# Optimization experiments

Measured on AMD Instinct MI355X. Metric: run time of the kernel, lower is better.

Reference implementation:

```python
import jax, jax.numpy as jnp
import numpy as np

B, D_IN = 32, 1024
A, N_PER = 4, 2048
N = A * N_PER
OUT_DIM = 11
THRESHOLD = 0.05
SELF_MASK, CROSS_MASK = 0.8, 0.1


def setup_inputs() -> dict:
    key = jax.random.key(0)
    ks = jax.random.split(key, 8)
    return {
        "x": jax.random.normal(ks[0], (B, D_IN), dtype=jnp.float32),
        "Z0": jax.random.normal(ks[1], (B, A, N_PER), dtype=jnp.float32),
        "receptors_w": jax.random.normal(ks[2], (N, D_IN), dtype=jnp.float32) * 0.02,
        "receptors_b": jax.random.normal(ks[3], (N,), dtype=jnp.float32) * 0.02,
        "synapses_w": jax.random.normal(ks[4], (N, N), dtype=jnp.float32) * 0.02,
        "synapses_b": jax.random.normal(ks[5], (N,), dtype=jnp.float32) * 0.02,
        "output_lobe_w": jax.random.normal(ks[6], (OUT_DIM, N), dtype=jnp.float32) * 0.02,
        "output_lobe_b": jax.random.normal(ks[7], (OUT_DIM,), dtype=jnp.float32) * 0.02,
        "area_idx": jnp.arange(N, dtype=jnp.int64).reshape(A, N_PER),
    }


def reference(x, Z0, receptors_w, receptors_b, synapses_w, synapses_b,
              output_lobe_w, output_lobe_b, area_idx):
    # area_idx: [A, n] partition of neurons into areas; perm: [N]
    perm = area_idx.reshape(-1)
    b = x.shape[0]

    # stimulus[i] = F.linear(x, receptors_w[idx_i], receptors_b[idx_i]),
    # computed for all areas at once then reshaped to per-area blocks.
    stim_flat = x @ receptors_w.T + receptors_b          # [B, N]
    stim = stim_flat[:, perm].reshape(b, A, N_PER)        # [B, A, n]

    # threshold gate per source area: |Z|.mean() > threshold (predicated)
    gate = (jnp.mean(jnp.abs(Z0), axis=(0, 2)) > THRESHOLD).astype(Z0.dtype)  # [A]

    # per-(out,in)-block synapse weights with clamped mask scale
    Wp = synapses_w[perm][:, perm].reshape(A, N_PER, A, N_PER)  # [A,n,A,n]
    scale = jnp.where(jnp.eye(A, dtype=bool), SELF_MASK, CROSS_MASK)  # [A,A]
    Weff = Wp * scale[:, None, :, None]

    # Z_next[out] = sum_in gate[in] * (Z[in] @ Weff[out,:,in,:].T) + gate[out]*bias[out]
    Zg = Z0 * gate[None, :, None]                         # [B, A, n]
    Znext = jnp.einsum('onam,bam->bon', Weff, Zg)         # [B, A, n]
    bias_blocks = synapses_b[perm].reshape(A, N_PER)      # diagonal-block bias
    Znext = Znext + gate[:, None] * bias_blocks           # fires with in==out gate

    Znew = jnp.tanh(Znext + stim)                         # [B, A, n]

    # scatter per-area state back into flat neuron order
    Z_flat = jnp.zeros((b, N), dtype=Znew.dtype).at[:, perm].set(Znew.reshape(b, N))

    raw = Z_flat @ output_lobe_w.T + output_lobe_b        # [B, 11]
    logits = raw[:, :10]
    out_gate = jax.nn.sigmoid(raw[:, 10])
    return logits, out_gate
```

## Files before the change

kernel.cpp:

```cpp
#include <hip/hip_runtime.h>
#include <math.h>

#define BATCH 32
#define DIN   1024
#define NAREA 4
#define NPER  2048
#define NTOT  8192
#define KC    256
#define RPB   16
#define SYN_CHUNKS 32
#define ALL_CHUNKS 36

typedef __attribute__((address_space(1))) const unsigned int gu32_t;
typedef __attribute__((address_space(3))) unsigned int su32_t;

__device__ __forceinline__ void load_lds16(const float* g, float* l) {
  __builtin_amdgcn_global_load_lds((gu32_t*)g, (su32_t*)l, 16, 0, 0);
}

__global__ void k_gate(const float* __restrict__ Z0, float* __restrict__ gsum) {
  const int a = blockIdx.x >> 3;
  const int slice = blockIdx.x & 7;
  const int tid = threadIdx.x;
  float s = 0.f;
#pragma unroll
  for (int it = 0; it < 8; ++it) {
    const int idx = it * 256 + tid;
    const int b = slice * 4 + (idx >> 9);
    const int n4 = idx & 511;
    const float4 z = *(const float4*)(Z0 + (size_t)b * NTOT + a * NPER + n4 * 4);
    s += fabsf(z.x) + fabsf(z.y) + fabsf(z.z) + fabsf(z.w);
  }
#pragma unroll
  for (int off = 32; off > 0; off >>= 1) s += __shfl_down(s, off);
  __shared__ float wsum[4];
  if ((tid & 63) == 0) wsum[tid >> 6] = s;
  __syncthreads();
  if (tid == 0) atomicAdd(&gsum[a], wsum[0] + wsum[1] + wsum[2] + wsum[3]);
}

__launch_bounds__(256, 2)
__global__ void k_main(const float* __restrict__ x,  const float* __restrict__ Z0,
                       const float* __restrict__ Rw, const float* __restrict__ rbias,
                       const float* __restrict__ Sw, const float* __restrict__ sbias,
                       const float* __restrict__ gsum, float* __restrict__ Zn) {
  __shared__ __align__(16) float zs[2][BATCH][KC];
  const int tid = threadIdx.x;
  const int w = tid >> 6, lane = tid & 63;
  const int r0 = blockIdx.x * RPB;
  const int o = r0 / NPER;
  const int rw0 = r0 + w * 4;

  float gate[NAREA], coeff[NAREA];
#pragma unroll
  for (int a = 0; a < NAREA; ++a) {
    gate[a] = (gsum[a] * (1.f / (BATCH * NPER)) > 0.05f) ? 1.f : 0.f;
    coeff[a] = gate[a] * ((a == o) ? 0.8f : 0.1f);
  }

  float acc[4][BATCH];
#pragma unroll
  for (int i = 0; i < 4; ++i)
#pragma unroll
    for (int b = 0; b < BATCH; ++b) acc[i][b] = 0.f;

  auto stage = [&](int kc, int buf) {
    const float* X; int stride, k0;
    if (kc < SYN_CHUNKS) { X = Z0; stride = NTOT; k0 = kc * KC; }
    else                 { X = x;  stride = DIN;  k0 = (kc - SYN_CHUNKS) * KC; }
#pragma unroll
    for (int i = 0; i < 8; ++i) {
      const int b = w * 8 + i;
      load_lds16(X + (size_t)b * stride + k0 + lane * 4, &zs[buf][b][0]);
    }
  };

  stage(0, 0);
  for (int kc = 0; kc < ALL_CHUNKS; ++kc) {
    const int buf = kc & 1;
    __syncthreads();
    if (kc + 1 < ALL_CHUNKS) stage(kc + 1, buf ^ 1);

    const float* Wm; int strideW, k0; float s;
    if (kc < SYN_CHUNKS) { Wm = Sw; strideW = NTOT; k0 = kc * KC; s = coeff[kc >> 3]; }
    else                 { Wm = Rw; strideW = DIN;  k0 = (kc - SYN_CHUNKS) * KC; s = 1.f; }

    float4 wv[4];
#pragma unroll
    for (int i = 0; i < 4; ++i)
      wv[i] = *(const float4*)(Wm + (size_t)(rw0 + i) * strideW + k0 + lane * 4);
#pragma unroll
    for (int i = 0; i < 4; ++i) { wv[i].x *= s; wv[i].y *= s; wv[i].z *= s; wv[i].w *= s; }

#pragma unroll
    for (int b = 0; b < BATCH; ++b) {
      const float4 z = *(const float4*)&zs[buf][b][lane * 4];
#pragma unroll
      for (int i = 0; i < 4; ++i) {
        acc[i][b] = fmaf(wv[i].x, z.x, acc[i][b]);
        acc[i][b] = fmaf(wv[i].y, z.y, acc[i][b]);
        acc[i][b] = fmaf(wv[i].z, z.z, acc[i][b]);
        acc[i][b] = fmaf(wv[i].w, z.w, acc[i][b]);
      }
    }
  }

  float (*L)[64] = reinterpret_cast<float (*)[64]>(&zs[0][0][0]);
  const float gate_o = gate[o];
#pragma unroll
  for (int h = 0; h < 2; ++h) {
    __syncthreads();
#pragma unroll
    for (int i = 0; i < 4; ++i)
#pragma unroll
      for (int bb = 0; bb < 16; ++bb)
        L[(w * 4 + i) * 16 + bb][lane] = acc[i][h * 16 + bb];
    __syncthreads();
#pragma unroll
    for (int step = 0; step < 6; ++step) {
      const int off = 32 >> step;
      for (int idx = tid; idx < (off << 8); idx += 256) {
        const int out = idx >> (5 - step);
        const int l = idx & (off - 1);
        L[out][l] += L[out][l + off];
      }
      __syncthreads();
    }
    const int r = r0 + (tid >> 4);
    const int b = h * 16 + (tid & 15);
    const float v = L[tid][0] + rbias[r] + gate_o * sbias[r];
    Zn[(size_t)r * BATCH + b] = tanhf(v);
  }
}

__global__ void k_proj(const float* __restrict__ Zn, const float* __restrict__ olw,
                       float* __restrict__ raw) {
  const int j = blockIdx.x >> 4;
  const int rs = blockIdx.x & 15;
  const int tid = threadIdx.x;
  const int b = tid & 31, stripe = tid >> 5;
  const int rbase = rs * 512 + stripe * 64;
  float a = 0.f;
#pragma unroll
  for (int rr = 0; rr < 64; ++rr) {
    const int r = rbase + rr;
    a = fmaf(olw[j * NTOT + r], Zn[(size_t)r * BATCH + b], a);
  }
  __shared__ float red[8][33];
  red[stripe][b] = a;
  __syncthreads();
  if (stripe == 0) {
    float v = 0.f;
#pragma unroll
    for (int s2 = 0; s2 < 8; ++s2) v += red[s2][b];
    atomicAdd(&raw[j * BATCH + b], v);
  }
}

__global__ void k_fin(const float* __restrict__ raw, const float* __restrict__ olb,
                      float* __restrict__ out) {
  const int t = threadIdx.x;
  if (t < 352) {
    const int j = t >> 5, b = t & 31;
    const float v = raw[j * BATCH + b] + olb[j];
    if (j < 10) out[b * 10 + j] = v;
    else        out[320 + b] = 1.f / (1.f + expf(-v));
  }
}

extern "C" void kernel_launch(void* const* d_in, const int* in_sizes, int n_in,
                              void* d_out, int out_size, void* d_ws, size_t ws_size,
                              hipStream_t stream) {
  const float* x    = (const float*)d_in[0];
  const float* Z0   = (const float*)d_in[1];
  const float* Rw   = (const float*)d_in[2];
  const float* rb_  = (const float*)d_in[3];
  const float* Sw   = (const float*)d_in[4];
  const float* sb_  = (const float*)d_in[5];
  const float* olw  = (const float*)d_in[6];
  const float* olb  = (const float*)d_in[7];

  float* ws   = (float*)d_ws;
  float* gsum = ws;
  float* raw  = ws + 8;
  float* Zn   = ws + 512;

  hipMemsetAsync(d_ws, 0, 512 * sizeof(float), stream);
  k_gate<<<32, 256, 0, stream>>>(Z0, gsum);
  k_main<<<NTOT / RPB, 256, 0, stream>>>(x, Z0, Rw, rb_, Sw, sb_, gsum, Zn);
  k_proj<<<11 * 16, 256, 0, stream>>>(Zn, olw, raw);
  k_fin<<<1, 384, 0, stream>>>(raw, olb, (float*)d_out);
}
```

Measured before the change: 430.6 us.

## Use bf16 MFMA for the fused synapse and receptor GEMM with pre-gated bf16 activations

Adds a prep kernel that applies the per-area gate to Z0, concatenates it with x, and converts the result to a bf16 activation matrix. The main kernel now runs 16x16x32 bf16 MFMAs on a 512-thread block, with each wave taking interleaved K chunks. Weights are scaled and converted to bf16 in registers, and the per-wave partial sums are reduced through LDS. This replaces the FP32 FMA loop and its LDS staging with matrix-core work, at the cost of bf16 precision and an extra kernel launch.

```diff
diff --git a/kernel.cpp b/kernel.cpp
--- a/kernel.cpp
+++ b/kernel.cpp
@@ -3,19 +3,18 @@
 
 #define BATCH 32
 #define DIN   1024
-#define NAREA 4
 #define NPER  2048
 #define NTOT  8192
-#define KC    256
-#define RPB   16
-#define SYN_CHUNKS 32
-#define ALL_CHUNKS 36
+#define KTOT  9216
+#define NCHUNK 288
 
-typedef __attribute__((address_space(1))) const unsigned int gu32_t;
-typedef __attribute__((address_space(3))) unsigned int su32_t;
+typedef __attribute__((ext_vector_type(8))) short short8;
+typedef __attribute__((ext_vector_type(4))) float f32x4;
 
-__device__ __forceinline__ void load_lds16(const float* g, float* l) {
-  __builtin_amdgcn_global_load_lds((gu32_t*)g, (su32_t*)l, 16, 0, 0);
+__device__ __forceinline__ unsigned short f2bf(float f) {
+  unsigned u = __float_as_uint(f);
+  u += 0x7FFF + ((u >> 16) & 1);
+  return (unsigned short)(u >> 16);
 }
 
 __global__ void k_gate(const float* __restrict__ Z0, float* __restrict__ gsum) {
@@ -39,98 +38,93 @@
   if (tid == 0) atomicAdd(&gsum[a], wsum[0] + wsum[1] + wsum[2] + wsum[3]);
 }
 
-__launch_bounds__(256, 2)
-__global__ void k_main(const float* __restrict__ x,  const float* __restrict__ Z0,
-                       const float* __restrict__ Rw, const float* __restrict__ rbias,
+__global__ void k_prep(const float* __restrict__ Z0, const float* __restrict__ x,
+                       const float* __restrict__ gsum, unsigned short* __restrict__ zg) {
+  const int idx = blockIdx.x * 256 + threadIdx.x;
+  const int b = idx / (KTOT / 4);
+  const int k = (idx % (KTOT / 4)) * 4;
+  float4 v; float g;
+  if (k < NTOT) {
+    v = *(const float4*)(Z0 + (size_t)b * NTOT + k);
+    g = (gsum[k >> 11] * (1.f / (BATCH * NPER)) > 0.05f) ? 1.f : 0.f;
+  } else {
+    v = *(const float4*)(x + (size_t)b * DIN + (k - NTOT));
+    g = 1.f;
+  }
+  ushort4 o;
+  o.x = f2bf(v.x * g); o.y = f2bf(v.y * g);
+  o.z = f2bf(v.z * g); o.w = f2bf(v.w * g);
+  *(ushort4*)(zg + (size_t)b * KTOT + k) = o;
+}
+
+__launch_bounds__(512, 4)
+__global__ void k_main(const float* __restrict__ Rw, const float* __restrict__ rbias,
                        const float* __restrict__ Sw, const float* __restrict__ sbias,
-                       const float* __restrict__ gsum, float* __restrict__ Zn) {
-  __shared__ __align__(16) float zs[2][BATCH][KC];
+                       const float* __restrict__ gsum, const unsigned short* __restrict__ zg,
+                       float* __restrict__ Zn) {
   const int tid = threadIdx.x;
   const int w = tid >> 6, lane = tid & 63;
-  const int r0 = blockIdx.x * RPB;
-  const int o = r0 / NPER;
-  const int rw0 = r0 + w * 4;
+  const int m = lane & 15, quad = lane >> 4;
+  const int r0 = blockIdx.x * 16;
+  const int o = r0 >> 11;
 
-  float gate[NAREA], coeff[NAREA];
+  float g[4];
 #pragma unroll
-  for (int a = 0; a < NAREA; ++a) {
-    gate[a] = (gsum[a] * (1.f / (BATCH * NPER)) > 0.05f) ? 1.f : 0.f;
-    coeff[a] = gate[a] * ((a == o) ? 0.8f : 0.1f);
+  for (int a = 0; a < 4; ++a)
+    g[a] = (gsum[a] * (1.f / (BATCH * NPER)) > 0.05f) ? 1.f : 0.f;
+  const float c0 = g[0] * ((o == 0) ? 0.8f : 0.1f);
+  const float c1 = g[1] * ((o == 1) ? 0.8f : 0.1f);
+  const float c2 = g[2] * ((o == 2) ? 0.8f : 0.1f);
+  const float c3 = g[3] * ((o == 3) ? 0.8f : 0.1f);
+
+  const float* swrow = Sw + (size_t)(r0 + m) * NTOT;
+  const float* rwrow = Rw + (size_t)(r0 + m) * DIN;
+  const unsigned short* zg0 = zg + (size_t)m * KTOT;
+  const unsigned short* zg1 = zg + (size_t)(m + 16) * KTOT;
+
+  f32x4 acc0 = {0.f, 0.f, 0.f, 0.f};
+  f32x4 acc1 = {0.f, 0.f, 0.f, 0.f};
+
+  for (int c = w; c < NCHUNK; c += 8) {
+    const int k0 = c * 32;
+    const float* ap; float s;
+    if (k0 < NTOT) {
+      ap = swrow + k0;
+      const int a = k0 >> 11;
+      s = (a == 0) ? c0 : (a == 1) ? c1 : (a == 2) ? c2 : c3;
+    } else {
+      ap = rwrow + (k0 - NTOT);
+      s = 1.f;
+    }
+    const float4 wv0 = *(const float4*)(ap + quad * 8);
+    const float4 wv1 = *(const float4*)(ap + quad * 8 + 4);
+    short8 af;
+    af[0] = (short)f2bf(wv0.x * s); af[1] = (short)f2bf(wv0.y * s);
+    af[2] = (short)f2bf(wv0.z * s); af[3] = (short)f2bf(wv0.w * s);
+    af[4] = (short)f2bf(wv1.x * s); af[5] = (short)f2bf(wv1.y * s);
+    af[6] = (short)f2bf(wv1.z * s); af[7] = (short)f2bf(wv1.w * s);
+    const short8 bf0 = *(const short8*)(zg0 + k0 + quad * 8);
+    const short8 bf1 = *(const short8*)(zg1 + k0 + quad * 8);
+    acc0 = __builtin_amdgcn_mfma_f32_16x16x32_bf16(af, bf0, acc0, 0, 0, 0);
+    acc1 = __builtin_amdgcn_mfma_f32_16x16x32_bf16(af, bf1, acc1, 0, 0, 0);
   }
 
-  float acc[4][BATCH];
+  __shared__ float red[8][2][16][16];
 #pragma unroll
-  for (int i = 0; i < 4; ++i)
+  for (int r = 0; r < 4; ++r) {
+    red[w][0][quad * 4 + r][m] = acc0[r];
+    red[w][1][quad * 4 + r][m] = acc1[r];
+  }
+  __syncthreads();
+  const int mrow = tid >> 5, n = tid & 31;
+  const int f = n >> 4, nn = n & 15;
+  float v = 0.f;
 #pragma unroll
-    for (int b = 0; b < BATCH; ++b) acc[i][b] = 0.f;
-
-  auto stage = [&](int kc, int buf) {
-    const float* X; int stride, k0;
-    if (kc < SYN_CHUNKS) { X = Z0; stride = NTOT; k0 = kc * KC; }
-    else                 { X = x;  stride = DIN;  k0 = (kc - SYN_CHUNKS) * KC; }
-#pragma unroll
-    for (int i = 0; i < 8; ++i) {
-      const int b = w * 8 + i;
-      load_lds16(X + (size_t)b * stride + k0 + lane * 4, &zs[buf][b][0]);
-    }
-  };
-
-  stage(0, 0);
-  for (int kc = 0; kc < ALL_CHUNKS; ++kc) {
-    const int buf = kc & 1;
-    __syncthreads();
-    if (kc + 1 < ALL_CHUNKS) stage(kc + 1, buf ^ 1);
-
-    const float* Wm; int strideW, k0; float s;
-    if (kc < SYN_CHUNKS) { Wm = Sw; strideW = NTOT; k0 = kc * KC; s = coeff[kc >> 3]; }
-    else                 { Wm = Rw; strideW = DIN;  k0 = (kc - SYN_CHUNKS) * KC; s = 1.f; }
-
-    float4 wv[4];
-#pragma unroll
-    for (int i = 0; i < 4; ++i)
-      wv[i] = *(const float4*)(Wm + (size_t)(rw0 + i) * strideW + k0 + lane * 4);
-#pragma unroll
-    for (int i = 0; i < 4; ++i) { wv[i].x *= s; wv[i].y *= s; wv[i].z *= s; wv[i].w *= s; }
-
-#pragma unroll
-    for (int b = 0; b < BATCH; ++b) {
-      const float4 z = *(const float4*)&zs[buf][b][lane * 4];
-#pragma unroll
-      for (int i = 0; i < 4; ++i) {
-        acc[i][b] = fmaf(wv[i].x, z.x, acc[i][b]);
-        acc[i][b] = fmaf(wv[i].y, z.y, acc[i][b]);
-        acc[i][b] = fmaf(wv[i].z, z.z, acc[i][b]);
-        acc[i][b] = fmaf(wv[i].w, z.w, acc[i][b]);
-      }
-    }
-  }
-
-  float (*L)[64] = reinterpret_cast<float (*)[64]>(&zs[0][0][0]);
-  const float gate_o = gate[o];
-#pragma unroll
-  for (int h = 0; h < 2; ++h) {
-    __syncthreads();
-#pragma unroll
-    for (int i = 0; i < 4; ++i)
-#pragma unroll
-      for (int bb = 0; bb < 16; ++bb)
-        L[(w * 4 + i) * 16 + bb][lane] = acc[i][h * 16 + bb];
-    __syncthreads();
-#pragma unroll
-    for (int step = 0; step < 6; ++step) {
-      const int off = 32 >> step;
-      for (int idx = tid; idx < (off << 8); idx += 256) {
-        const int out = idx >> (5 - step);
-        const int l = idx & (off - 1);
-        L[out][l] += L[out][l + off];
-      }
-      __syncthreads();
-    }
-    const int r = r0 + (tid >> 4);
-    const int b = h * 16 + (tid & 15);
-    const float v = L[tid][0] + rbias[r] + gate_o * sbias[r];
-    Zn[(size_t)r * BATCH + b] = tanhf(v);
-  }
+  for (int ww = 0; ww < 8; ++ww) v += red[ww][f][mrow][nn];
+  const int r = r0 + mrow;
+  const float gate_o = (o == 0) ? g[0] : (o == 1) ? g[1] : (o == 2) ? g[2] : g[3];
+  v += rbias[r] + gate_o * sbias[r];
+  Zn[(size_t)r * BATCH + n] = tanhf(v);
 }
 
 __global__ void k_proj(const float* __restrict__ Zn, const float* __restrict__ olw,
@@ -184,10 +178,12 @@
   float* gsum = ws;
   float* raw  = ws + 8;
   float* Zn   = ws + 512;
+  unsigned short* zg = (unsigned short*)(ws + 512 + NTOT * BATCH);
 
   hipMemsetAsync(d_ws, 0, 512 * sizeof(float), stream);
   k_gate<<<32, 256, 0, stream>>>(Z0, gsum);
-  k_main<<<NTOT / RPB, 256, 0, stream>>>(x, Z0, Rw, rb_, Sw, sb_, gsum, Zn);
+  k_prep<<<BATCH * KTOT / 1024, 256, 0, stream>>>(Z0, x, gsum, zg);
+  k_main<<<NTOT / 16, 512, 0, stream>>>(Rw, rb_, Sw, sb_, gsum, zg, Zn);
   k_proj<<<11 * 16, 256, 0, stream>>>(Zn, olw, raw);
   k_fin<<<1, 384, 0, stream>>>(raw, olb, (float*)d_out);
 }
```

After: 421.2 us. 2.2% less time.
